# Performance work log

Hardware: AMD Instinct MI355X
Metric: run time of the kernel (lower is better)

## Reference

```python
import jax, jax.numpy as jnp
import numpy as np

O = 64        # group-rep dimension (U_y, U_x are O x O)
C_OUT = 96    # output channel blocks
C_IN = 96     # input channel blocks
SOFTNESS = 0.0


def _build_structure():
    """Build the Schur block structure: 24 2x2 rotation blocks (8 distinct
    angles x 3 copies) + 16 1x1 blocks (+1/-1). sigma_y == sigma_x, so the
    mask marks matching blocks and rows/cols index matched 2x2 sub-blocks."""
    blocks = []
    angles = [0.15 * (k + 1) for k in range(8)]
    for a in angles:
        for _ in range(3):
            blocks.append(('R', round(a, 6)))
    for k in range(16):
        blocks.append(('D', 1.0 if k % 2 == 0 else -1.0))
    dims = [2 if t == 'R' else 1 for t, _ in blocks]
    n = sum(dims)
    assert n == O
    mask = np.zeros((n, n), np.float32)
    rows, cols = [], []
    yc = 0
    for (ti, vi), di in zip(blocks, dims):
        xc = 0
        for (tj, vj), dj in zip(blocks, dims):
            if di == dj and ti == tj and vi == vj:
                mask[yc:yc + di, xc:xc + dj] = 1.0
                if di == 2:
                    rows += [yc, yc, yc + 1, yc + 1]
                    cols += [xc, xc + 1, xc, xc + 1]
            xc += dj
        yc += di
    return mask, np.asarray(rows, np.int32), np.asarray(cols, np.int32)


def setup_inputs() -> dict:
    key = jax.random.key(0)
    k1, k2, k3 = jax.random.split(key, 3)
    W = jax.random.normal(k1, (C_OUT * O, C_IN * O), jnp.float32)
    # Orthogonal Schur bases via QR of Gaussian matrices
    U_y = jnp.linalg.qr(jax.random.normal(k2, (O, O), jnp.float32))[0]
    U_x = jnp.linalg.qr(jax.random.normal(k3, (O, O), jnp.float32))[0]
    mask_np, rows_np, cols_np = _build_structure()
    return {
        'W': W,
        'U_y': U_y,
        'U_x': U_x,
        'mask': jnp.asarray(mask_np),
        'block_rows': jnp.asarray(rows_np),
        'block_cols': jnp.asarray(cols_np),
    }


def reference(W, U_y, U_x, mask, block_rows, block_cols):
    o = U_y.shape[0]
    i = U_x.shape[0]
    c_out = W.shape[-2] // o
    c_in = W.shape[-1] // i
    # _to_blocks: (c_out*o, c_in*i) -> (c_out, c_in, o, i)
    Wb = W.reshape(c_out, o, c_in, i).transpose(0, 2, 1, 3)
    # W' = U_y.T @ W @ U_x, then apply sparsity mask
    Wp = jnp.einsum('po,bcpq,qk->bcok', U_y, Wb, U_x) * mask
    # Gather matched 2x2 sub-blocks: (c_out, c_in, num_blocks, 2, 2)
    nb = block_rows.shape[0] // 4
    g = Wp[..., block_rows, block_cols].reshape(c_out, c_in, nb, 2, 2)
    alpha = (g[..., 0, 0] + g[..., 1, 1]) * 0.5
    beta = (g[..., 0, 1] - g[..., 1, 0]) * 0.5
    hard = jnp.stack([jnp.stack([alpha, beta], axis=-1),
                      jnp.stack([-beta, alpha], axis=-1)], axis=-2)
    soft = SOFTNESS * g + (1.0 - SOFTNESS) * hard
    # Scatter symmetrized blocks back (index pairs are unique)
    Wp = Wp.at[..., block_rows, block_cols].set(soft.reshape(c_out, c_in, -1))
    # W_out = U_y @ W'_proj @ U_x.T
    out_b = jnp.einsum('op,bcpq,kq->bcok', U_y, Wp, U_x)
    # _from_blocks: (c_out, c_in, o, i) -> (c_out*o, c_in*i)
    return out_b.transpose(0, 2, 1, 3).reshape(c_out * o, c_in * i)
```

## Files before the change

### kernel.cpp

```cpp
#include <hip/hip_runtime.h>


#define NB  96
#define NW  6144
#define LDP 72

typedef _Float16 f16;
typedef _Float16 half8 __attribute__((ext_vector_type(8)));
typedef _Float16 half4 __attribute__((ext_vector_type(4)));
typedef float    f32x4 __attribute__((ext_vector_type(4)));

__device__ __forceinline__ half8 ld8(const f16* p) {
    return *reinterpret_cast<const half8*>(p);
}
__device__ __forceinline__ float xor1(float x) {
    return __builtin_bit_cast(float,
        __builtin_amdgcn_mov_dpp(__builtin_bit_cast(int, x), 0xB1, 0xF, 0xF, true));
}

__global__ void prep_u(const float* __restrict__ Uy, const float* __restrict__ Ux,
                       f16* __restrict__ Upack) {
    int idx = blockIdx.x * 256 + threadIdx.x;
    int r = idx >> 6, c = idx & 63;
    int p = ((r >> 4) * 2 + (c >> 5)) * 512 + (((c & 31) >> 3) * 16 + (r & 15)) * 8 + (c & 7);
    Upack[0 * 4096 + p] = (f16)Ux[c * 64 + r];
    Upack[1 * 4096 + p] = (f16)Uy[c * 64 + r];
    Upack[2 * 4096 + p] = (f16)Ux[r * 64 + c];
    Upack[3 * 4096 + p] = (f16)Uy[r * 64 + c];
}

__global__ __launch_bounds__(256, 4)
void schur_fused(const float* __restrict__ W,
                 const f16* __restrict__ Upack,
                 float* __restrict__ out) {
    __shared__ f16 lds[4][64 * LDP];

    const int t  = threadIdx.x;
    const int w  = t >> 6;
    const int l  = t & 63;
    const int lr = l & 15;
    const int lg = l >> 4;

    const int blk = blockIdx.x * 4 + w;
    const int bo  = blk / NB;
    const int bc  = blk % NB;

    f16* buf = lds[w];

    const f16* UxTi = Upack;
    const f16* UyTi = Upack + 4096;
    const f16* Uxi  = Upack + 8192;
    const f16* Uyi  = Upack + 12288;

    {
        const int cr = l >> 4;
        const int cc = l & 15;
        const float* srcb = W + (size_t)(bo * 64 + cr) * NW + bc * 64 + cc * 4;
        f16* dstb = buf + cr * LDP + cc * 4;
        float4 vc[4], vn[4];
#pragma unroll
        for (int q = 0; q < 4; ++q)
            vn[q] = *reinterpret_cast<const float4*>(srcb + (size_t)(q * 16) * NW);
#pragma unroll
        for (int grp = 0; grp < 4; ++grp) {
#pragma unroll
            for (int q = 0; q < 4; ++q) vc[q] = vn[q];
            if (grp < 3) {
#pragma unroll
                for (int q = 0; q < 4; ++q)
                    vn[q] = *reinterpret_cast<const float4*>(
                        srcb + (size_t)((grp + 1) * 4 + q * 16) * NW);
            }
#pragma unroll
            for (int q = 0; q < 4; ++q) {
                half4 h = { (f16)vc[q].x, (f16)vc[q].y, (f16)vc[q].z, (f16)vc[q].w };
                *reinterpret_cast<half4*>(dstb + (q * 4 + grp) * 4 * LDP) = h;
            }
        }
    }

    f32x4 acc[4][4];
    half8 b[4][2];

    auto ldbI = [&](const f16* img) {
#pragma unroll
        for (int ct = 0; ct < 4; ++ct) {
            b[ct][0] = ld8(img + (ct * 2 + 0) * 512 + l * 8);
            b[ct][1] = ld8(img + (ct * 2 + 1) * 512 + l * 8);
        }
    };
    auto mmAL = [&]() {
#pragma unroll
        for (int rt = 0; rt < 4; ++rt) {
            const f16* ar = buf + (rt * 16 + lr) * LDP + lg * 8;
            half8 a0 = ld8(ar), a1 = ld8(ar + 32);
#pragma unroll
            for (int ct = 0; ct < 4; ++ct) {
                f32x4 d = {0.f, 0.f, 0.f, 0.f};
                d = __builtin_amdgcn_mfma_f32_16x16x32_f16(a0, b[ct][0], d, 0, 0, 0);
                d = __builtin_amdgcn_mfma_f32_16x16x32_f16(a1, b[ct][1], d, 0, 0, 0);
                acc[rt][ct] = d;
            }
        }
    };
    auto mmAI = [&](const f16* img) {
#pragma unroll
        for (int rt = 0; rt < 4; ++rt) {
            half8 a0 = ld8(img + (rt * 2 + 0) * 512 + l * 8);
            half8 a1 = ld8(img + (rt * 2 + 1) * 512 + l * 8);
#pragma unroll
            for (int ct = 0; ct < 4; ++ct) {
                f32x4 d = {0.f, 0.f, 0.f, 0.f};
                d = __builtin_amdgcn_mfma_f32_16x16x32_f16(a0, b[ct][0], d, 0, 0, 0);
                d = __builtin_amdgcn_mfma_f32_16x16x32_f16(a1, b[ct][1], d, 0, 0, 0);
                acc[rt][ct] = d;
            }
        }
    };
    auto ldbL = [&]() {
#pragma unroll
        for (int ct = 0; ct < 4; ++ct) {
            const f16* br = buf + (ct * 16 + lr) * LDP + lg * 8;
            b[ct][0] = ld8(br);
            b[ct][1] = ld8(br + 32);
        }
    };
    auto wrT = [&]() {
#pragma unroll
        for (int rt = 0; rt < 4; ++rt)
#pragma unroll
            for (int ct = 0; ct < 4; ++ct) {
                f32x4 v = acc[rt][ct];
                half4 h = { (f16)v[0], (f16)v[1], (f16)v[2], (f16)v[3] };
                *reinterpret_cast<half4*>(buf + (ct * 16 + lr) * LDP + rt * 16 + lg * 4) = h;
            }
    };

    ldbI(UxTi); mmAL(); wrT();
    ldbI(UyTi); mmAL();

#pragma unroll
    for (int rt = 0; rt < 4; ++rt) {
        const int kbase = rt * 16 + lg * 4;
#pragma unroll
        for (int ct = 0; ct < 4; ++ct) {
            const int o = ct * 16 + lr;
            const float s = (o & 1) ? -1.f : 1.f;
            const bool oeven = ((o & 1) == 0);
#pragma unroll
            for (int p = 0; p < 2; ++p) {
                const int k0 = kbase + 2 * p;
                float x0 = acc[rt][ct][2 * p];
                float x1 = acc[rt][ct][2 * p + 1];
                float t0 = xor1(x0);
                float t1 = xor1(x1);
                const bool Ract = (o < 48) && (k0 < 48) &&
                                  ((o * 43 >> 8) == (k0 * 43 >> 8));
                const bool Dact = (o >= 48) && (k0 >= 48);
                float r0v = 0.5f * (x0 + s * t1);
                float r1v = 0.5f * (x1 - s * t0);
                float d0 = oeven ? x0 : 0.f;
                float d1 = oeven ? 0.f : x1;
                acc[rt][ct][2 * p]     = Ract ? r0v : (Dact ? d0 : 0.f);
                acc[rt][ct][2 * p + 1] = Ract ? r1v : (Dact ? d1 : 0.f);
            }
        }
    }

    wrT();
    ldbI(Uxi); mmAL(); wrT();
    ldbL(); mmAI(Uyi);

    {
        float* ob = out + (size_t)(bo * 64 + lg * 4) * NW + bc * 64 + lr;
#pragma unroll
        for (int rt = 0; rt < 4; ++rt)
#pragma unroll
            for (int i = 0; i < 4; ++i) {
                float* rp = ob + (size_t)(rt * 16 + i) * NW;
#pragma unroll
                for (int ct = 0; ct < 4; ++ct)
                    rp[ct * 16] = acc[rt][ct][i];
            }
    }
}

extern "C" void kernel_launch(void* const* d_in, const int* in_sizes, int n_in,
                              void* d_out, int out_size, void* d_ws, size_t ws_size,
                              hipStream_t stream) {
    const float* W  = (const float*)d_in[0];
    const float* Uy = (const float*)d_in[1];
    const float* Ux = (const float*)d_in[2];

    f16*   Upack = (f16*)d_ws;
    float* o     = (float*)d_out;

    prep_u<<<dim3(16), 256, 0, stream>>>(Uy, Ux, Upack);
    schur_fused<<<dim3(NB * NB / 4), 256, 0, stream>>>(W, Upack, o);
}
```

Baseline: 72.90 us.

## Process four blocks per wave with software-pipelined W prefetch

Each wave now loops over four consecutive 64x64 blocks instead of one, and the grid shrinks by a factor of four. The next block's first half of W is prefetched into registers during the current block's compute, and the second half is loaded while the first matmul rows run, to hide global load latency. Launch bounds drop to 3 waves per SIMD to make room for the extra prefetch registers. In exchange the kernel has fewer waves in flight and a longer serial chain per wave.

```diff
diff --git a/kernel.cpp b/kernel.cpp
--- a/kernel.cpp
+++ b/kernel.cpp
@@ -12,6 +12,9 @@
 
 __device__ __forceinline__ half8 ld8(const f16* p) {
     return *reinterpret_cast<const half8*>(p);
+}
+__device__ __forceinline__ float4 ldf4(const float* p) {
+    return *reinterpret_cast<const float4*>(p);
 }
 __device__ __forceinline__ float xor1(float x) {
     return __builtin_bit_cast(float,
@@ -29,7 +32,7 @@
     Upack[3 * 4096 + p] = (f16)Uy[r * 64 + c];
 }
 
-__global__ __launch_bounds__(256, 4)
+__global__ __launch_bounds__(256, 3)
 void schur_fused(const float* __restrict__ W,
                  const f16* __restrict__ Upack,
                  float* __restrict__ out) {
@@ -41,9 +44,7 @@
     const int lr = l & 15;
     const int lg = l >> 4;
 
-    const int blk = blockIdx.x * 4 + w;
-    const int bo  = blk / NB;
-    const int bc  = blk % NB;
+    const int wgid = blockIdx.x * 4 + w;
 
     f16* buf = lds[w];
 
@@ -52,32 +53,8 @@
     const f16* Uxi  = Upack + 8192;
     const f16* Uyi  = Upack + 12288;
 
-    {
-        const int cr = l >> 4;
-        const int cc = l & 15;
-        const float* srcb = W + (size_t)(bo * 64 + cr) * NW + bc * 64 + cc * 4;
-        f16* dstb = buf + cr * LDP + cc * 4;
-        float4 vc[4], vn[4];
-#pragma unroll
-        for (int q = 0; q < 4; ++q)
-            vn[q] = *reinterpret_cast<const float4*>(srcb + (size_t)(q * 16) * NW);
-#pragma unroll
-        for (int grp = 0; grp < 4; ++grp) {
-#pragma unroll
-            for (int q = 0; q < 4; ++q) vc[q] = vn[q];
-            if (grp < 3) {
-#pragma unroll
-                for (int q = 0; q < 4; ++q)
-                    vn[q] = *reinterpret_cast<const float4*>(
-                        srcb + (size_t)((grp + 1) * 4 + q * 16) * NW);
-            }
-#pragma unroll
-            for (int q = 0; q < 4; ++q) {
-                half4 h = { (f16)vc[q].x, (f16)vc[q].y, (f16)vc[q].z, (f16)vc[q].w };
-                *reinterpret_cast<half4*>(dstb + (q * 4 + grp) * 4 * LDP) = h;
-            }
-        }
-    }
+    const int cr = lg;
+    const int cc = lr;
 
     f32x4 acc[4][4];
     half8 b[4][2];
@@ -89,11 +66,22 @@
             b[ct][1] = ld8(img + (ct * 2 + 1) * 512 + l * 8);
         }
     };
-    auto mmAL = [&]() {
+    auto mmRT = [&](int rt) {
+        const f16* ar = buf + (rt * 16 + lr) * LDP + lg * 8;
+        half8 a0 = ld8(ar), a1 = ld8(ar + 32);
+#pragma unroll
+        for (int ct = 0; ct < 4; ++ct) {
+            f32x4 d = {0.f, 0.f, 0.f, 0.f};
+            d = __builtin_amdgcn_mfma_f32_16x16x32_f16(a0, b[ct][0], d, 0, 0, 0);
+            d = __builtin_amdgcn_mfma_f32_16x16x32_f16(a1, b[ct][1], d, 0, 0, 0);
+            acc[rt][ct] = d;
+        }
+    };
+    auto mmAI = [&](const f16* img) {
 #pragma unroll
         for (int rt = 0; rt < 4; ++rt) {
-            const f16* ar = buf + (rt * 16 + lr) * LDP + lg * 8;
-            half8 a0 = ld8(ar), a1 = ld8(ar + 32);
+            half8 a0 = ld8(img + (rt * 2 + 0) * 512 + l * 8);
+            half8 a1 = ld8(img + (rt * 2 + 1) * 512 + l * 8);
 #pragma unroll
             for (int ct = 0; ct < 4; ++ct) {
                 f32x4 d = {0.f, 0.f, 0.f, 0.f};
@@ -103,20 +91,6 @@
             }
         }
     };
-    auto mmAI = [&](const f16* img) {
-#pragma unroll
-        for (int rt = 0; rt < 4; ++rt) {
-            half8 a0 = ld8(img + (rt * 2 + 0) * 512 + l * 8);
-            half8 a1 = ld8(img + (rt * 2 + 1) * 512 + l * 8);
-#pragma unroll
-            for (int ct = 0; ct < 4; ++ct) {
-                f32x4 d = {0.f, 0.f, 0.f, 0.f};
-                d = __builtin_amdgcn_mfma_f32_16x16x32_f16(a0, b[ct][0], d, 0, 0, 0);
-                d = __builtin_amdgcn_mfma_f32_16x16x32_f16(a1, b[ct][1], d, 0, 0, 0);
-                acc[rt][ct] = d;
-            }
-        }
-    };
     auto ldbL = [&]() {
 #pragma unroll
         for (int ct = 0; ct < 4; ++ct) {
@@ -136,52 +110,107 @@
             }
     };
 
-    ldbI(UxTi); mmAL(); wrT();
-    ldbI(UyTi); mmAL();
-
-#pragma unroll
-    for (int rt = 0; rt < 4; ++rt) {
-        const int kbase = rt * 16 + lg * 4;
-#pragma unroll
-        for (int ct = 0; ct < 4; ++ct) {
-            const int o = ct * 16 + lr;
-            const float s = (o & 1) ? -1.f : 1.f;
-            const bool oeven = ((o & 1) == 0);
-#pragma unroll
-            for (int p = 0; p < 2; ++p) {
-                const int k0 = kbase + 2 * p;
-                float x0 = acc[rt][ct][2 * p];
-                float x1 = acc[rt][ct][2 * p + 1];
-                float t0 = xor1(x0);
-                float t1 = xor1(x1);
-                const bool Ract = (o < 48) && (k0 < 48) &&
-                                  ((o * 43 >> 8) == (k0 * 43 >> 8));
-                const bool Dact = (o >= 48) && (k0 >= 48);
-                float r0v = 0.5f * (x0 + s * t1);
-                float r1v = 0.5f * (x1 - s * t0);
-                float d0 = oeven ? x0 : 0.f;
-                float d1 = oeven ? 0.f : x1;
-                acc[rt][ct][2 * p]     = Ract ? r0v : (Dact ? d0 : 0.f);
-                acc[rt][ct][2 * p + 1] = Ract ? r1v : (Dact ? d1 : 0.f);
+    float4 pf[8];
+
+    {
+        const int blk = wgid * 4;
+        const int bo = blk / NB, bc = blk % NB;
+        const float* srcb = W + (size_t)(bo * 64 + cr) * NW + bc * 64 + cc * 4;
+#pragma unroll
+        for (int i = 0; i < 8; ++i)
+            pf[i] = ldf4(srcb + (size_t)(4 * (i & 3) + 16 * (i >> 2)) * NW);
+    }
+
+#pragma unroll 1
+    for (int j = 0; j < 4; ++j) {
+        const int blk = wgid * 4 + j;
+        const int bo = blk / NB, bc = blk % NB;
+        const float* srcb = W + (size_t)(bo * 64 + cr) * NW + bc * 64 + cc * 4;
+        f16* dstb = buf + cr * LDP + cc * 4;
+
+        float4 sh[8];
+#pragma unroll
+        for (int i = 0; i < 8; ++i)
+            sh[i] = ldf4(srcb + (size_t)(4 * (i & 3) + 16 * (2 + (i >> 2))) * NW);
+
+#pragma unroll
+        for (int i = 0; i < 8; ++i) {
+            float4 v = pf[i];
+            half4 h = { (f16)v.x, (f16)v.y, (f16)v.z, (f16)v.w };
+            *reinterpret_cast<half4*>(dstb + (((i >> 2) * 4 + (i & 3)) * 4) * LDP) = h;
+        }
+
+        ldbI(UxTi);
+        mmRT(0); mmRT(1);
+
+#pragma unroll
+        for (int i = 0; i < 8; ++i) {
+            float4 v = sh[i];
+            half4 h = { (f16)v.x, (f16)v.y, (f16)v.z, (f16)v.w };
+            *reinterpret_cast<half4*>(dstb + (((2 + (i >> 2)) * 4 + (i & 3)) * 4) * LDP) = h;
+        }
+
+        if (j < 3) {
+            const int nblk = blk + 1;
+            const int nbo = nblk / NB, nbc = nblk % NB;
+            const float* nsrc = W + (size_t)(nbo * 64 + cr) * NW + nbc * 64 + cc * 4;
+#pragma unroll
+            for (int i = 0; i < 8; ++i)
+                pf[i] = ldf4(nsrc + (size_t)(4 * (i & 3) + 16 * (i >> 2)) * NW);
+        }
+
+        mmRT(2); mmRT(3);
+        wrT();
+
+        ldbI(UyTi);
+        mmRT(0); mmRT(1); mmRT(2); mmRT(3);
+
+#pragma unroll
+        for (int rt = 0; rt < 4; ++rt) {
+            const int kbase = rt * 16 + lg * 4;
+#pragma unroll
+            for (int ct = 0; ct < 4; ++ct) {
+                const int o = ct * 16 + lr;
+                const float s = (o & 1) ? -1.f : 1.f;
+                const bool oeven = ((o & 1) == 0);
+#pragma unroll
+                for (int p = 0; p < 2; ++p) {
+                    const int k0 = kbase + 2 * p;
+                    float x0 = acc[rt][ct][2 * p];
+                    float x1 = acc[rt][ct][2 * p + 1];
+                    float t0 = xor1(x0);
+                    float t1 = xor1(x1);
+                    const bool Ract = (o < 48) && (k0 < 48) &&
+                                      ((o * 43 >> 8) == (k0 * 43 >> 8));
+                    const bool Dact = (o >= 48) && (k0 >= 48);
+                    float r0v = 0.5f * (x0 + s * t1);
+                    float r1v = 0.5f * (x1 - s * t0);
+                    float d0 = oeven ? x0 : 0.f;
+                    float d1 = oeven ? 0.f : x1;
+                    acc[rt][ct][2 * p]     = Ract ? r0v : (Dact ? d0 : 0.f);
+                    acc[rt][ct][2 * p + 1] = Ract ? r1v : (Dact ? d1 : 0.f);
+                }
             }
         }
-    }
-
-    wrT();
-    ldbI(Uxi); mmAL(); wrT();
-    ldbL(); mmAI(Uyi);
-
-    {
-        float* ob = out + (size_t)(bo * 64 + lg * 4) * NW + bc * 64 + lr;
-#pragma unroll
-        for (int rt = 0; rt < 4; ++rt)
-#pragma unroll
-            for (int i = 0; i < 4; ++i) {
-                float* rp = ob + (size_t)(rt * 16 + i) * NW;
-#pragma unroll
-                for (int ct = 0; ct < 4; ++ct)
-                    rp[ct * 16] = acc[rt][ct][i];
-            }
+
+        wrT();
+        ldbI(Uxi);
+        mmRT(0); mmRT(1); mmRT(2); mmRT(3);
+        wrT();
+        ldbL(); mmAI(Uyi);
+
+        {
+            float* ob = out + (size_t)(bo * 64 + lg * 4) * NW + bc * 64 + lr;
+#pragma unroll
+            for (int rt = 0; rt < 4; ++rt)
+#pragma unroll
+                for (int i = 0; i < 4; ++i) {
+                    float* rp = ob + (size_t)(rt * 16 + i) * NW;
+#pragma unroll
+                    for (int ct = 0; ct < 4; ++ct)
+                        rp[ct * 16] = acc[rt][ct][i];
+                }
+        }
     }
 }
 
@@ -196,5 +225,5 @@
     float* o     = (float*)d_out;
 
     prep_u<<<dim3(16), 256, 0, stream>>>(Uy, Ux, Upack);
-    schur_fused<<<dim3(NB * NB / 4), 256, 0, stream>>>(W, Upack, o);
-}
+    schur_fused<<<dim3(NB * NB / 16), 256, 0, stream>>>(W, Upack, o);
+}
```

After: 147.4 us. +102.1%, slower.
